# Performance work log

Measured on AMD Instinct MI355X. Metric: run time of the kernel, lower is better.

The kernel has to match this reference:

```python
import jax, jax.numpy as jnp
import numpy as np

# ThrusterLagConfig constants
PWM_CENTER = 7.5
PWM_HALF_RANGE = 2.5
DEADZONE = 0.05
SAT_GAIN = 2.0
TAU_INIT = 0.08
TAU_MIN = 0.01
DT = 0.01
N_THRUSTERS = 8


def setup_inputs() -> dict:
    key = jax.random.key(0)
    k_u, = jax.random.split(key, 1)
    B, L, C = 512, 8192, N_THRUSTERS
    # raw PWM duty in [5, 10]
    u_seq = jax.random.uniform(k_u, (B, L, C), dtype=jnp.float32, minval=5.0, maxval=10.0)
    # learnable tau parameter, initialized as in __init__:
    # tau0 = clamp(tau_init - tau_min, 1e-6); p0 = log(expm1(tau0))
    tau0 = max(TAU_INIT - TAU_MIN, 1e-6)
    p0 = float(np.log(np.expm1(tau0)))
    tau_param = jnp.full((C,), p0, dtype=jnp.float32)
    return {"u_seq": u_seq, "tau_param": tau_param}


def reference(u_seq, tau_param):
    # PWM duty -> [-1, 1]
    u_unit = (u_seq - PWM_CENTER) / PWM_HALF_RANGE
    # deadzone: softshrink(u, lambd) = sign(u) * max(|u| - lambd, 0)
    u_dz = jnp.sign(u_unit) * jnp.maximum(jnp.abs(u_unit) - DEADZONE, 0.0)
    # smooth saturation
    u_nl = jnp.tanh(SAT_GAIN * u_dz)  # (B, L, C)

    # a = exp(-dt / tau), tau = softplus(p) + tau_min, per channel (C,)
    tau = jax.nn.softplus(tau_param) + TAU_MIN
    a = jnp.exp(-DT / tau)  # (C,)

    # first-order lag IIR: u_eff[k] = a * u_eff[k-1] + (1 - a) * u_nl[k]
    # u0_eff defaults to u_nl[:, 0, :]
    u0 = u_nl[:, 0, :]  # (B, C)

    def step(u_prev, uk):
        u_new = a * u_prev + (1.0 - a) * uk
        return u_new, u_new

    xs = jnp.moveaxis(u_nl, 1, 0)  # (L, B, C)
    _, ys = jax.lax.scan(step, u0, xs)
    return jnp.moveaxis(ys, 0, 1)  # (B, L, C)
```

## Files before the change

kernel.cpp:

```cpp
#include <hip/hip_runtime.h>
#include <math.h>


typedef float v4f __attribute__((ext_vector_type(4)));

constexpr int kB     = 512;
constexpr int kL     = 8192;
constexpr int kC     = 8;
constexpr int kOut   = 256;
constexpr int kChunk = 128;
constexpr int kSegs  = kL / kOut;
constexpr int kNCh   = kOut / kChunk;

constexpr float kDT     = 0.01f;
constexpr float kTauMin = 0.01f;

__device__ __forceinline__ float rfl(float x) {
    return __int_as_float(__builtin_amdgcn_readfirstlane(__float_as_int(x)));
}

__device__ __forceinline__ float softplus_f(float p) {
    return fmaxf(p, 0.0f) + log1pf(__expf(-fabsf(p)));
}

__device__ __forceinline__ v4f u_nl4(v4f u) {
    v4f s = u * 0.8f - 6.0f;
    v4f x;
    #pragma unroll
    for (int i = 0; i < 4; ++i) {
        float cl = fminf(fmaxf(s[i], -0.1f), 0.1f);
        x[i] = s[i] - cl;
    }
    v4f t = x * x;
    v4f p = t * -0.0072811f + 0.070674f;
    p = t * p - 0.297221f;
    p = t * p + 0.996226f;
    return x * p;
}

template<int CTRL>
__device__ __forceinline__ float dpp_mov(float v) {
    return __int_as_float(__builtin_amdgcn_update_dpp(
        0, __float_as_int(v), CTRL, 0xF, 0xF, false));
}
#define DPP_SHR(d)   (0x110 | (d))
#define DPP_BC15     0x142
#define DPP_BC31     0x143

__device__ __forceinline__ float bperm(int addr, float v) {
    return __int_as_float(__builtin_amdgcn_ds_bpermute(addr, __float_as_int(v)));
}

__global__ __launch_bounds__(256, 2) void scan_seg(const float* __restrict__ u,
                                                   const float* __restrict__ tp,
                                                   float* __restrict__ out) {
    const int lane = threadIdx.x & 63;
    const int seg  = blockIdx.x * 4 + (threadIdx.x >> 6);
    const int r    = seg >> 5;
    const int sq   = seg & (kSegs - 1);

    float a2[kC], a4[kC], a8[kC], a16[kC];
    float a[kC], om[kC], ia2[kC], Ms[kC];
    v4f D0, D1, W15a, W15b, W31a, W31b;
    #pragma unroll
    for (int c = 0; c < kC; ++c) {
        float tau = softplus_f(tp[c]) + kTauMin;
        float lna = -kDT / tau;
        float av  = __expf(lna);
        float v2 = av * av, v4 = v2 * v2, v8 = v4 * v4;
        a[c]   = rfl(av);
        om[c]  = rfl(1.0f - av);
        a2[c]  = rfl(v2);
        a4[c]  = rfl(v4);
        a8[c]  = rfl(v8);
        a16[c] = rfl(v8 * v8);
        ia2[c] = rfl(1.0f / v2);
        Ms[c]  = rfl(__expf(lna * (float)kChunk));
        float d   = __expf(lna * (float)(2 * lane));
        float w15 = (lane & 16)  ? __expf(lna * (float)(2 * ((lane & 15) + 1))) : 0.0f;
        float w31 = (lane >= 32) ? __expf(lna * (float)(2 * (lane - 31)))       : 0.0f;
        if (c < 4) { D0[c] = d; W15a[c] = w15; W31a[c] = w31; }
        else       { D1[c-4] = d; W15b[c-4] = w15; W31b[c-4] = w31; }
    }
    v4f A0 = {a[0],a[1],a[2],a[3]},     A1 = {a[4],a[5],a[6],a[7]};
    v4f O0 = {om[0],om[1],om[2],om[3]}, O1 = {om[4],om[5],om[6],om[7]};
    v4f V0 = {ia2[0],ia2[1],ia2[2],ia2[3]}, V1 = {ia2[4],ia2[5],ia2[6],ia2[7]};
    v4f M0 = {Ms[0],Ms[1],Ms[2],Ms[3]}, M1 = {Ms[4],Ms[5],Ms[6],Ms[7]};

    const float* base  = u   + (size_t)r * kL * kC;
    float*       obase = out + (size_t)r * kL * kC;

    v4f K0, K1;
    int start, nch, wfrom;
    if (sq == 0) {
        start = 0; nch = kNCh; wfrom = 0;
        K0 = u_nl4(*(const v4f*)(base));
        K1 = u_nl4(*(const v4f*)(base + 4));
    } else {
        start = sq * kOut - kChunk;
        nch = kNCh + 1; wfrom = 1;
        K0 = (v4f){0,0,0,0};
        K1 = (v4f){0,0,0,0};
    }

    const int addr63 = 63 << 2;

    const float* tb0 = base + (size_t)(start + lane * 2) * kC;
    v4f x0 = *(const v4f*)(tb0);
    v4f x1 = *(const v4f*)(tb0 + 4);
    v4f x2 = *(const v4f*)(tb0 + 8);
    v4f x3 = *(const v4f*)(tb0 + 12);

    for (int ch = 0; ch < nch; ++ch) {
        const size_t off = (size_t)(start + ch * kChunk + lane * 2) * kC;

        v4f n0 = u_nl4(x0), n1 = u_nl4(x1), n2 = u_nl4(x2), n3 = u_nl4(x3);
        v4f l00 = O0 * n0;
        v4f l01 = O1 * n1;
        v4f l10 = A0 * l00 + O0 * n2;
        v4f l11 = A1 * l01 + O1 * n3;

        if (ch + 1 < nch) {
            const float* nb = base + (off + (size_t)kChunk * kC);
            x0 = *(const v4f*)(nb);
            x1 = *(const v4f*)(nb + 4);
            x2 = *(const v4f*)(nb + 8);
            x3 = *(const v4f*)(nb + 12);
        }

        float I[kC];
        #pragma unroll
        for (int c = 0; c < 4; ++c) { I[c] = l10[c]; I[c + 4] = l11[c]; }
        #pragma unroll
        for (int c = 0; c < kC; ++c) I[c] = fmaf(a2[c],  dpp_mov<DPP_SHR(1)>(I[c]), I[c]);
        #pragma unroll
        for (int c = 0; c < kC; ++c) I[c] = fmaf(a4[c],  dpp_mov<DPP_SHR(2)>(I[c]), I[c]);
        #pragma unroll
        for (int c = 0; c < kC; ++c) I[c] = fmaf(a8[c],  dpp_mov<DPP_SHR(4)>(I[c]), I[c]);
        #pragma unroll
        for (int c = 0; c < kC; ++c) I[c] = fmaf(a16[c], dpp_mov<DPP_SHR(8)>(I[c]), I[c]);
        #pragma unroll
        for (int c = 0; c < 4; ++c) {
            I[c]     = fmaf(W15a[c], dpp_mov<DPP_BC15>(I[c]),     I[c]);
            I[c + 4] = fmaf(W15b[c], dpp_mov<DPP_BC15>(I[c + 4]), I[c + 4]);
        }
        #pragma unroll
        for (int c = 0; c < 4; ++c) {
            I[c]     = fmaf(W31a[c], dpp_mov<DPP_BC31>(I[c]),     I[c]);
            I[c + 4] = fmaf(W31b[c], dpp_mov<DPP_BC31>(I[c + 4]), I[c + 4]);
        }

        v4f Tt0, Tt1;
        #pragma unroll
        for (int c = 0; c < 4; ++c) {
            Tt0[c] = bperm(addr63, I[c]);
            Tt1[c] = bperm(addr63, I[c + 4]);
        }
        v4f I0 = {I[0], I[1], I[2], I[3]};
        v4f I1 = {I[4], I[5], I[6], I[7]};
        v4f E0 = (I0 - l10) * V0;
        v4f E1 = (I1 - l11) * V1;

        if (ch >= wfrom) {
            float* ob = obase + off;
            v4f C0  = D0 * K0 + E0;
            v4f C1  = D1 * K1 + E1;
            v4f cy0 = A0 * C0;
            v4f cy1 = A1 * C1;
            *(v4f*)(ob)      = l00 + cy0;
            *(v4f*)(ob + 4)  = l01 + cy1;
            *(v4f*)(ob + 8)  = A0 * cy0 + l10;
            *(v4f*)(ob + 12) = A1 * cy1 + l11;
        }

        K0 = M0 * K0 + Tt0;
        K1 = M1 * K1 + Tt1;
    }
}

extern "C" void kernel_launch(void* const* d_in, const int* in_sizes, int n_in,
                              void* d_out, int out_size, void* d_ws, size_t ws_size,
                              hipStream_t stream) {
    const float* u  = (const float*)d_in[0];
    const float* tp = (const float*)d_in[1];
    float* out = (float*)d_out;

    scan_seg<<<(kB * kSegs) / 4, 256, 0, stream>>>(u, tp, out);
}
```

Before: 61.84 us.

## Double segment length and fully unroll chunks with two-deep prefetch

Each wave's output segment grows from 256 to 512 timesteps. This halves the number of segments and cuts the redundant 128-step warm-up overhead from 1/2 to 1/4 of the processed data. The chunk loop is fully unrolled via a macro with two register buffers, so loads run two chunks ahead to hide more memory latency. In exchange, half as many waves are launched and register pressure rises from holding two input chunks.

```diff
diff --git a/kernel.cpp b/kernel.cpp
--- a/kernel.cpp
+++ b/kernel.cpp
@@ -7,10 +7,9 @@
 constexpr int kB     = 512;
 constexpr int kL     = 8192;
 constexpr int kC     = 8;
-constexpr int kOut   = 256;
+constexpr int kOut   = 512;
 constexpr int kChunk = 128;
 constexpr int kSegs  = kL / kOut;
-constexpr int kNCh   = kOut / kChunk;
 
 constexpr float kDT     = 0.01f;
 constexpr float kTauMin = 0.01f;
@@ -51,12 +50,70 @@
     return __int_as_float(__builtin_amdgcn_ds_bpermute(addr, __float_as_int(v)));
 }
 
+#define PROC(X0, X1, X2, X3, CH, DO_PF, DO_ST)                                  \
+    {                                                                           \
+        v4f n0 = u_nl4(X0), n1 = u_nl4(X1), n2 = u_nl4(X2), n3 = u_nl4(X3);     \
+        if (DO_PF) {                                                            \
+            const float* nb = base +                                            \
+                (size_t)(start + ((CH) + 2) * kChunk + lane * 2) * kC;          \
+            X0 = *(const v4f*)(nb);                                             \
+            X1 = *(const v4f*)(nb + 4);                                         \
+            X2 = *(const v4f*)(nb + 8);                                         \
+            X3 = *(const v4f*)(nb + 12);                                        \
+        }                                                                       \
+        v4f l00 = O0 * n0;                                                      \
+        v4f l01 = O1 * n1;                                                      \
+        v4f l10 = A0 * l00 + O0 * n2;                                           \
+        v4f l11 = A1 * l01 + O1 * n3;                                           \
+        float I[kC];                                                            \
+        for (int c = 0; c < 4; ++c) { I[c] = l10[c]; I[c + 4] = l11[c]; }       \
+        for (int c = 0; c < kC; ++c)                                            \
+            I[c] = fmaf(a2[c], dpp_mov<DPP_SHR(1)>(I[c]), I[c]);                \
+        for (int c = 0; c < kC; ++c)                                            \
+            I[c] = fmaf(a4[c], dpp_mov<DPP_SHR(2)>(I[c]), I[c]);                \
+        for (int c = 0; c < kC; ++c)                                            \
+            I[c] = fmaf(a8[c], dpp_mov<DPP_SHR(4)>(I[c]), I[c]);                \
+        for (int c = 0; c < kC; ++c)                                            \
+            I[c] = fmaf(a16[c], dpp_mov<DPP_SHR(8)>(I[c]), I[c]);               \
+        for (int c = 0; c < 4; ++c) {                                           \
+            I[c]     = fmaf(W15a[c], dpp_mov<DPP_BC15>(I[c]),     I[c]);        \
+            I[c + 4] = fmaf(W15b[c], dpp_mov<DPP_BC15>(I[c + 4]), I[c + 4]);    \
+        }                                                                       \
+        for (int c = 0; c < 4; ++c) {                                           \
+            I[c]     = fmaf(W31a[c], dpp_mov<DPP_BC31>(I[c]),     I[c]);        \
+            I[c + 4] = fmaf(W31b[c], dpp_mov<DPP_BC31>(I[c + 4]), I[c + 4]);    \
+        }                                                                       \
+        v4f Tt0, Tt1;                                                           \
+        for (int c = 0; c < 4; ++c) {                                           \
+            Tt0[c] = bperm(addr63, I[c]);                                       \
+            Tt1[c] = bperm(addr63, I[c + 4]);                                   \
+        }                                                                       \
+        v4f I0 = {I[0], I[1], I[2], I[3]};                                      \
+        v4f I1 = {I[4], I[5], I[6], I[7]};                                      \
+        v4f E0 = (I0 - l10) * V0;                                               \
+        v4f E1 = (I1 - l11) * V1;                                               \
+        if (DO_ST) {                                                            \
+            float* ob = obase +                                                 \
+                (size_t)(start + (CH) * kChunk + lane * 2) * kC;                \
+            v4f C0  = D0 * K0 + E0;                                             \
+            v4f C1  = D1 * K1 + E1;                                             \
+            v4f cy0 = A0 * C0;                                                  \
+            v4f cy1 = A1 * C1;                                                  \
+            *(v4f*)(ob)      = l00 + cy0;                                       \
+            *(v4f*)(ob + 4)  = l01 + cy1;                                       \
+            *(v4f*)(ob + 8)  = A0 * cy0 + l10;                                  \
+            *(v4f*)(ob + 12) = A1 * cy1 + l11;                                  \
+        }                                                                       \
+        K0 = M0 * K0 + Tt0;                                                     \
+        K1 = M1 * K1 + Tt1;                                                     \
+    }
+
 __global__ __launch_bounds__(256, 2) void scan_seg(const float* __restrict__ u,
                                                    const float* __restrict__ tp,
                                                    float* __restrict__ out) {
     const int lane = threadIdx.x & 63;
     const int seg  = blockIdx.x * 4 + (threadIdx.x >> 6);
-    const int r    = seg >> 5;
+    const int r    = seg >> 4;
     const int sq   = seg & (kSegs - 1);
 
     float a2[kC], a4[kC], a8[kC], a16[kC];
@@ -90,91 +147,42 @@
     const float* base  = u   + (size_t)r * kL * kC;
     float*       obase = out + (size_t)r * kL * kC;
 
+    const int addr63 = 63 << 2;
+
     v4f K0, K1;
-    int start, nch, wfrom;
+    int start;
     if (sq == 0) {
-        start = 0; nch = kNCh; wfrom = 0;
+        start = 0;
         K0 = u_nl4(*(const v4f*)(base));
         K1 = u_nl4(*(const v4f*)(base + 4));
     } else {
         start = sq * kOut - kChunk;
-        nch = kNCh + 1; wfrom = 1;
-        K0 = (v4f){0,0,0,0};
-        K1 = (v4f){0,0,0,0};
+        K0 = (v4f){0, 0, 0, 0};
+        K1 = (v4f){0, 0, 0, 0};
     }
 
-    const int addr63 = 63 << 2;
+    const float* pA = base + (size_t)(start + lane * 2) * kC;
+    const float* pB = pA + (size_t)kChunk * kC;
+    v4f xa0 = *(const v4f*)(pA);
+    v4f xa1 = *(const v4f*)(pA + 4);
+    v4f xa2 = *(const v4f*)(pA + 8);
+    v4f xa3 = *(const v4f*)(pA + 12);
+    v4f xb0 = *(const v4f*)(pB);
+    v4f xb1 = *(const v4f*)(pB + 4);
+    v4f xb2 = *(const v4f*)(pB + 8);
+    v4f xb3 = *(const v4f*)(pB + 12);
 
-    const float* tb0 = base + (size_t)(start + lane * 2) * kC;
-    v4f x0 = *(const v4f*)(tb0);
-    v4f x1 = *(const v4f*)(tb0 + 4);
-    v4f x2 = *(const v4f*)(tb0 + 8);
-    v4f x3 = *(const v4f*)(tb0 + 12);
-
-    for (int ch = 0; ch < nch; ++ch) {
-        const size_t off = (size_t)(start + ch * kChunk + lane * 2) * kC;
-
-        v4f n0 = u_nl4(x0), n1 = u_nl4(x1), n2 = u_nl4(x2), n3 = u_nl4(x3);
-        v4f l00 = O0 * n0;
-        v4f l01 = O1 * n1;
-        v4f l10 = A0 * l00 + O0 * n2;
-        v4f l11 = A1 * l01 + O1 * n3;
-
-        if (ch + 1 < nch) {
-            const float* nb = base + (off + (size_t)kChunk * kC);
-            x0 = *(const v4f*)(nb);
-            x1 = *(const v4f*)(nb + 4);
-            x2 = *(const v4f*)(nb + 8);
-            x3 = *(const v4f*)(nb + 12);
-        }
-
-        float I[kC];
-        #pragma unroll
-        for (int c = 0; c < 4; ++c) { I[c] = l10[c]; I[c + 4] = l11[c]; }
-        #pragma unroll
-        for (int c = 0; c < kC; ++c) I[c] = fmaf(a2[c],  dpp_mov<DPP_SHR(1)>(I[c]), I[c]);
-        #pragma unroll
-        for (int c = 0; c < kC; ++c) I[c] = fmaf(a4[c],  dpp_mov<DPP_SHR(2)>(I[c]), I[c]);
-        #pragma unroll
-        for (int c = 0; c < kC; ++c) I[c] = fmaf(a8[c],  dpp_mov<DPP_SHR(4)>(I[c]), I[c]);
-        #pragma unroll
-        for (int c = 0; c < kC; ++c) I[c] = fmaf(a16[c], dpp_mov<DPP_SHR(8)>(I[c]), I[c]);
-        #pragma unroll
-        for (int c = 0; c < 4; ++c) {
-            I[c]     = fmaf(W15a[c], dpp_mov<DPP_BC15>(I[c]),     I[c]);
-            I[c + 4] = fmaf(W15b[c], dpp_mov<DPP_BC15>(I[c + 4]), I[c + 4]);
-        }
-        #pragma unroll
-        for (int c = 0; c < 4; ++c) {
-            I[c]     = fmaf(W31a[c], dpp_mov<DPP_BC31>(I[c]),     I[c]);
-            I[c + 4] = fmaf(W31b[c], dpp_mov<DPP_BC31>(I[c + 4]), I[c + 4]);
-        }
-
-        v4f Tt0, Tt1;
-        #pragma unroll
-        for (int c = 0; c < 4; ++c) {
-            Tt0[c] = bperm(addr63, I[c]);
-            Tt1[c] = bperm(addr63, I[c + 4]);
-        }
-        v4f I0 = {I[0], I[1], I[2], I[3]};
-        v4f I1 = {I[4], I[5], I[6], I[7]};
-        v4f E0 = (I0 - l10) * V0;
-        v4f E1 = (I1 - l11) * V1;
-
-        if (ch >= wfrom) {
-            float* ob = obase + off;
-            v4f C0  = D0 * K0 + E0;
-            v4f C1  = D1 * K1 + E1;
-            v4f cy0 = A0 * C0;
-            v4f cy1 = A1 * C1;
-            *(v4f*)(ob)      = l00 + cy0;
-            *(v4f*)(ob + 4)  = l01 + cy1;
-            *(v4f*)(ob + 8)  = A0 * cy0 + l10;
-            *(v4f*)(ob + 12) = A1 * cy1 + l11;
-        }
-
-        K0 = M0 * K0 + Tt0;
-        K1 = M1 * K1 + Tt1;
+    if (sq == 0) {
+        PROC(xa0, xa1, xa2, xa3, 0, true,  true);
+        PROC(xb0, xb1, xb2, xb3, 1, true,  true);
+        PROC(xa0, xa1, xa2, xa3, 2, false, true);
+        PROC(xb0, xb1, xb2, xb3, 3, false, true);
+    } else {
+        PROC(xa0, xa1, xa2, xa3, 0, true,  false);
+        PROC(xb0, xb1, xb2, xb3, 1, true,  true);
+        PROC(xa0, xa1, xa2, xa3, 2, true,  true);
+        PROC(xb0, xb1, xb2, xb3, 3, false, true);
+        PROC(xa0, xa1, xa2, xa3, 4, false, true);
     }
 }
 
```

Result: faster. 57.45 us (-7.1%).
